# Performance work log

Hardware: AMD Instinct MI355X
Metric: run time of the kernel (lower is better)

Reference implementation:

```python
import jax, jax.numpy as jnp
import numpy as np

EMBED = 1024
FF = 4096
HEADS = 16
HEAD_SIZE = EMBED // HEADS


def setup_inputs() -> dict:
    key = jax.random.key(0)
    ks = jax.random.split(key, 12)
    s = 0.02
    inp = {
        "x": jax.random.normal(ks[0], (2, 2048, EMBED), dtype=jnp.float32),
        "Wq": jax.random.normal(ks[1], (EMBED, EMBED), dtype=jnp.float32) * s,
        "bq": jnp.zeros((EMBED,), jnp.float32),
        "Wk": jax.random.normal(ks[2], (EMBED, EMBED), dtype=jnp.float32) * s,
        "bk": jnp.zeros((EMBED,), jnp.float32),
        "Wv": jax.random.normal(ks[3], (EMBED, EMBED), dtype=jnp.float32) * s,
        "bv": jnp.zeros((EMBED,), jnp.float32),
        "Wo": jax.random.normal(ks[4], (EMBED, EMBED), dtype=jnp.float32) * s,
        "bo": jnp.zeros((EMBED,), jnp.float32),
        "W1": jax.random.normal(ks[5], (EMBED, FF), dtype=jnp.float32) * s,
        "b1": jnp.zeros((FF,), jnp.float32),
        "W2": jax.random.normal(ks[6], (FF, EMBED), dtype=jnp.float32) * s,
        "b2": jnp.zeros((EMBED,), jnp.float32),
        "ln1_g": jnp.ones((EMBED,), jnp.float32),
        "ln1_b": jnp.zeros((EMBED,), jnp.float32),
        "ln2_g": jnp.ones((EMBED,), jnp.float32),
        "ln2_b": jnp.zeros((EMBED,), jnp.float32),
    }
    return inp


def _layernorm(x, g, b, eps=1e-5):
    mu = jnp.mean(x, axis=-1, keepdims=True)
    var = jnp.var(x, axis=-1, keepdims=True)
    return (x - mu) * jax.lax.rsqrt(var + eps) * g + b


def _attn(x, Wq, bq, Wk, bk, Wv, bv, Wo, bo):
    B, S, E = x.shape
    q = (x @ Wq + bq).reshape(B, S, HEADS, HEAD_SIZE)
    k = (x @ Wk + bk).reshape(B, S, HEADS, HEAD_SIZE)
    v = (x @ Wv + bv).reshape(B, S, HEADS, HEAD_SIZE)
    # full (non-causal) attention, scores materialized as in the original
    att = jnp.einsum('bqhd,bkhd->bhqk', q, k) / jnp.sqrt(jnp.float32(HEAD_SIZE))
    att = jax.nn.softmax(att, axis=-1)
    out = jnp.einsum('bhqk,bkhd->bqhd', att, v).reshape(B, S, E)
    return out @ Wo + bo


def reference(x, Wq, bq, Wk, bk, Wv, bv, Wo, bo, W1, b1, W2, b2,
              ln1_g, ln1_b, ln2_g, ln2_b):
    x = x + _attn(_layernorm(x, ln1_g, ln1_b), Wq, bq, Wk, bk, Wv, bv, Wo, bo)
    h = _layernorm(x, ln2_g, ln2_b)
    x = x + (jax.nn.gelu(h @ W1 + b1) @ W2 + b2)
    return x
```

## Files before the change

kernel.cpp:

```cpp
#include <hip/hip_runtime.h>

typedef __bf16 bf16;
typedef __bf16 bf16x8 __attribute__((ext_vector_type(8)));
typedef __bf16 bf16x4 __attribute__((ext_vector_type(4)));
typedef float f32x4 __attribute__((ext_vector_type(4)));

#define EMBED 1024
#define FFDIM 4096
#define HEADS 16
#define HD 64
#define SEQ 2048
#define BATCH 2
#define TOKENS (BATCH * SEQ)
#define MB (1u << 20)


__device__ __forceinline__ void gld16(const void* g, void* l) {
  __builtin_amdgcn_global_load_lds(
      (const __attribute__((address_space(1))) void*)g,
      (__attribute__((address_space(3))) void*)l, 16, 0, 0);
}

__device__ __forceinline__ float gelu_f(float x) {
  float u = 0.7978845608028654f * (x + 0.044715f * x * x * x);
  float t = tanhf(u);
  return 0.5f * x * (1.0f + t);
}

__device__ __forceinline__ void xcd_tiles(int nx, int& tx, int& ty) {
  int lid = blockIdx.x + nx * blockIdx.y;
  tx = (lid >> 3) % nx;
  ty = ((lid / (8 * nx)) << 3) | (lid & 7);
}

__global__ __launch_bounds__(256) void transpose_cast(const float* __restrict__ in,
                                                      bf16* __restrict__ out,
                                                      int R, int C) {
  __shared__ float t[32][33];
  int bx = blockIdx.x * 32;
  int by = blockIdx.y * 32;
  int tx = threadIdx.x & 31;
  int ty = threadIdx.x >> 5;
#pragma unroll
  for (int i = 0; i < 32; i += 8)
    t[ty + i][tx] = in[(size_t)(by + ty + i) * C + bx + tx];
  __syncthreads();
#pragma unroll
  for (int i = 0; i < 32; i += 8)
    out[(size_t)(bx + ty + i) * R + by + tx] = (bf16)t[tx][ty + i];
}

__global__ __launch_bounds__(256) void ln_kernel(const float* __restrict__ x,
                                                 const float* __restrict__ g,
                                                 const float* __restrict__ b,
                                                 bf16* __restrict__ out) {
  int tok = blockIdx.x;
  int tid = threadIdx.x;
  const float4* xv = (const float4*)(x + (size_t)tok * EMBED);
  float4 v = xv[tid];
  float s = v.x + v.y + v.z + v.w;
  float s2 = v.x * v.x + v.y * v.y + v.z * v.z + v.w * v.w;
#pragma unroll
  for (int off = 32; off >= 1; off >>= 1) {
    s += __shfl_xor(s, off, 64);
    s2 += __shfl_xor(s2, off, 64);
  }
  __shared__ float ps[4], ps2[4];
  int w = tid >> 6;
  if ((tid & 63) == 0) { ps[w] = s; ps2[w] = s2; }
  __syncthreads();
  s = ps[0] + ps[1] + ps[2] + ps[3];
  s2 = ps2[0] + ps2[1] + ps2[2] + ps2[3];
  float mu = s * (1.0f / EMBED);
  float var = s2 * (1.0f / EMBED) - mu * mu;
  float r = rsqrtf(var + 1e-5f);
  float4 gg = ((const float4*)g)[tid];
  float4 bb = ((const float4*)b)[tid];
  bf16x4 o;
  o[0] = (bf16)((v.x - mu) * r * gg.x + bb.x);
  o[1] = (bf16)((v.y - mu) * r * gg.y + bb.y);
  o[2] = (bf16)((v.z - mu) * r * gg.z + bb.z);
  o[3] = (bf16)((v.w - mu) * r * gg.w + bb.w);
  ((bf16x4*)(out + (size_t)tok * EMBED))[tid] = o;
}

template <int MODE>
__global__ __launch_bounds__(256) void gemm_bt(const bf16* __restrict__ A,
                                               const bf16* __restrict__ BT,
                                               const float* __restrict__ bias,
                                               void* __restrict__ out,
                                               int M, int N, int K,
                                               const float* __restrict__ bias2,
                                               const float* __restrict__ bias3,
                                               void* __restrict__ out2,
                                               void* __restrict__ out3) {
  __shared__ bf16 ldsA[128 * 64];
  __shared__ bf16 ldsB[128 * 64];
  int tid = threadIdx.x;
  int wave = tid >> 6, lane = tid & 63;
  int lquad = lane >> 4, l15 = lane & 15;
  int wm = wave >> 1, wn = wave & 1;
  int tileM = blockIdx.y * 128, tileN = blockIdx.x * 128;

  f32x4 acc[4][4];
#pragma unroll
  for (int i = 0; i < 4; i++)
#pragma unroll
    for (int j = 0; j < 4; j++) acc[i][j] = (f32x4){0.f, 0.f, 0.f, 0.f};

  int srow = lane >> 3;
  int sch = lane & 7;

  for (int k0 = 0; k0 < K; k0 += 64) {
    __syncthreads();
#pragma unroll
    for (int c = 0; c < 4; c++) {
      int base = wave * 32 + c * 8;
      int row = base + srow;
      int ch = sch ^ (row & 7);
      gld16(&A[(size_t)(tileM + row) * K + k0 + ch * 8], &ldsA[base * 64]);
      gld16(&BT[(size_t)(tileN + row) * K + k0 + ch * 8], &ldsB[base * 64]);
    }
    __syncthreads();

    bf16x8 aF[2][4], bF[2][4];
#pragma unroll
    for (int ks = 0; ks < 2; ks++) {
#pragma unroll
      for (int i = 0; i < 4; i++) {
        int R = wm * 64 + i * 16 + l15;
        int ch = (ks * 4 + lquad) ^ (R & 7);
        aF[ks][i] = *(const bf16x8*)&ldsA[R * 64 + ch * 8];
      }
#pragma unroll
      for (int j = 0; j < 4; j++) {
        int R = wn * 64 + j * 16 + l15;
        int ch = (ks * 4 + lquad) ^ (R & 7);
        bF[ks][j] = *(const bf16x8*)&ldsB[R * 64 + ch * 8];
      }
    }
#pragma unroll
    for (int i = 0; i < 4; i++)
#pragma unroll
      for (int j = 0; j < 4; j++)
#pragma unroll
        for (int ks = 0; ks < 2; ks++)
          acc[i][j] = __builtin_amdgcn_mfma_f32_16x16x32_bf16(aF[ks][i], bF[ks][j], acc[i][j], 0, 0, 0);
  }

  int r0 = tileM + wm * 64;
  int c0 = tileN + wn * 64;
#pragma unroll
  for (int i = 0; i < 4; i++) {
#pragma unroll
    for (int j = 0; j < 4; j++) {
      int col = c0 + j * 16 + l15;
      float bv;
      if (MODE == 4) {
        int sel = col >> 10, cc = col & 1023;
        bv = (sel == 0 ? bias : sel == 1 ? bias2 : bias3)[cc];
      } else {
        bv = bias[col];
      }
#pragma unroll
      for (int r = 0; r < 4; r++) {
        int row = r0 + i * 16 + lquad * 4 + r;
        float v = acc[i][j][r] + bv;
        if (MODE == 0) {
          ((bf16*)out)[(size_t)row * N + col] = (bf16)v;
        } else if (MODE == 3) {
          ((bf16*)out)[(size_t)row * N + col] = (bf16)gelu_f(v);
        } else {
          int sel = col >> 10, cc = col & 1023;
          if (sel == 0) {
            ((bf16*)out)[(size_t)row * EMBED + cc] = (bf16)v;
          } else if (sel == 1) {
            ((bf16*)out2)[(size_t)row * EMBED + cc] = (bf16)v;
          } else {
            int bb = row >> 11, s = row & (SEQ - 1);
            ((bf16*)out3)[((size_t)(bb * EMBED + cc)) * SEQ + s] = (bf16)v;
          }
        }
      }
    }
  }
}

__global__ __launch_bounds__(256) void gemm_bt64(const bf16* __restrict__ A,
                                                 const bf16* __restrict__ BT,
                                                 const float* __restrict__ bias,
                                                 const float* __restrict__ res,
                                                 float* __restrict__ out,
                                                 int M, int N, int K) {
  __shared__ bf16 ldsA[128 * 64];
  __shared__ bf16 ldsB[64 * 64];
  int tid = threadIdx.x;
  int wave = tid >> 6, lane = tid & 63;
  int lquad = lane >> 4, l15 = lane & 15;
  int wm = wave >> 1, wn = wave & 1;
  int txs, tys;
  xcd_tiles(N >> 6, txs, tys);
  int tileM = tys * 128, tileN = txs * 64;

  f32x4 acc[4][2];
#pragma unroll
  for (int i = 0; i < 4; i++)
#pragma unroll
    for (int j = 0; j < 2; j++) acc[i][j] = (f32x4){0.f, 0.f, 0.f, 0.f};

  int srow = lane >> 3;
  int sch = lane & 7;

  for (int k0 = 0; k0 < K; k0 += 64) {
    __syncthreads();
#pragma unroll
    for (int c = 0; c < 4; c++) {
      int base = wave * 32 + c * 8;
      int row = base + srow;
      int ch = sch ^ (row & 7);
      gld16(&A[(size_t)(tileM + row) * K + k0 + ch * 8], &ldsA[base * 64]);
    }
#pragma unroll
    for (int c = 0; c < 2; c++) {
      int base = wave * 16 + c * 8;
      int row = base + srow;
      int ch = sch ^ (row & 7);
      gld16(&BT[(size_t)(tileN + row) * K + k0 + ch * 8], &ldsB[base * 64]);
    }
    __syncthreads();

    bf16x8 aF[2][4], bF[2][2];
#pragma unroll
    for (int ks = 0; ks < 2; ks++) {
#pragma unroll
      for (int i = 0; i < 4; i++) {
        int R = wm * 64 + i * 16 + l15;
        int ch = (ks * 4 + lquad) ^ (R & 7);
        aF[ks][i] = *(const bf16x8*)&ldsA[R * 64 + ch * 8];
      }
#pragma unroll
      for (int j = 0; j < 2; j++) {
        int R = wn * 32 + j * 16 + l15;
        int ch = (ks * 4 + lquad) ^ (R & 7);
        bF[ks][j] = *(const bf16x8*)&ldsB[R * 64 + ch * 8];
      }
    }
#pragma unroll
    for (int i = 0; i < 4; i++)
#pragma unroll
      for (int j = 0; j < 2; j++)
#pragma unroll
        for (int ks = 0; ks < 2; ks++)
          acc[i][j] = __builtin_amdgcn_mfma_f32_16x16x32_bf16(aF[ks][i], bF[ks][j], acc[i][j], 0, 0, 0);
  }

  int r0 = tileM + wm * 64;
  int c0 = tileN + wn * 32;
#pragma unroll
  for (int i = 0; i < 4; i++) {
#pragma unroll
    for (int j = 0; j < 2; j++) {
      int col = c0 + j * 16 + l15;
      float bv = bias[col];
#pragma unroll
      for (int r = 0; r < 4; r++) {
        int row = r0 + i * 16 + lquad * 4 + r;
        out[(size_t)row * N + col] = acc[i][j][r] + bv + res[(size_t)row * N + col];
      }
    }
  }
}

__global__ __launch_bounds__(256) void attn_kernel(const bf16* __restrict__ q,
                                                   const bf16* __restrict__ k,
                                                   const bf16* __restrict__ vT,
                                                   bf16* __restrict__ o) {
  int lid = blockIdx.x;
  int qb = (lid >> 3) & 31;
  int g = (lid & 7) | ((lid >> 8) << 3);
  int h = g & 15, b = g >> 4;
  int tid = threadIdx.x;
  int w = tid >> 6, lane = tid & 63;
  int lquad = lane >> 4, l15 = lane & 15;

  __shared__ bf16 ldsK[128 * 64];
  __shared__ bf16 ldsV[64 * 128];
  __shared__ bf16 ldsP[4][16 * 136];

  int qrow = b * SEQ + qb * 64 + w * 16 + l15;
  bf16x8 qB[2];
  qB[0] = *(const bf16x8*)&q[(size_t)qrow * EMBED + h * HD + 0 + lquad * 8];
  qB[1] = *(const bf16x8*)&q[(size_t)qrow * EMBED + h * HD + 32 + lquad * 8];

  f32x4 O[4];
#pragma unroll
  for (int j = 0; j < 4; j++) O[j] = (f32x4){0.f, 0.f, 0.f, 0.f};
  float m = -1e30f, lsum = 0.f;
  const float C2 = 0.18033688011112042f;

  for (int kb = 0; kb < SEQ; kb += 128) {
    __syncthreads();
#pragma unroll
    for (int c = 0; c < 4; c++) {
      int base = w * 32 + c * 8;
      int row = base + (lane >> 3);
      int ch = (lane & 7) ^ (row & 7);
      gld16(&k[(size_t)(b * SEQ + kb + row) * EMBED + h * HD + ch * 8],
            &ldsK[base * 64]);
    }
#pragma unroll
    for (int c = 0; c < 4; c++) {
      int base = w * 16 + c * 4;
      int row = base + (lane >> 4);
      int ch = (lane & 15) ^ (row & 7);
      gld16(&vT[(size_t)(b * EMBED + h * HD + row) * SEQ + kb + ch * 8],
            &ldsV[base * 128]);
    }
    __syncthreads();

    f32x4 st[8];
#pragma unroll
    for (int t = 0; t < 8; t++) {
      st[t] = (f32x4){0.f, 0.f, 0.f, 0.f};
#pragma unroll
      for (int ks = 0; ks < 2; ks++) {
        int R = t * 16 + l15;
        int ch = (ks * 4 + lquad) ^ (R & 7);
        bf16x8 kA = *(const bf16x8*)&ldsK[R * 64 + ch * 8];
        st[t] = __builtin_amdgcn_mfma_f32_16x16x32_bf16(kA, qB[ks], st[t], 0, 0, 0);
      }
    }

    float mt = fmaxf(fmaxf(st[0][0], st[0][1]), fmaxf(st[0][2], st[0][3]));
#pragma unroll
    for (int t = 1; t < 8; t++) {
      float a0 = fmaxf(st[t][0], st[t][1]);
      float a1 = fmaxf(st[t][2], st[t][3]);
      mt = fmaxf(mt, fmaxf(a0, a1));
    }
    mt = fmaxf(mt, __shfl_xor(mt, 16, 64));
    mt = fmaxf(mt, __shfl_xor(mt, 32, 64));
    float mn = fmaxf(m, mt);
    float alpha = __builtin_amdgcn_exp2f((m - mn) * C2);
    m = mn;
    float mc2 = m * C2;

    float rs = 0.f;
#pragma unroll
    for (int t = 0; t < 8; t++)
#pragma unroll
      for (int r = 0; r < 4; r++) {
        st[t][r] = __builtin_amdgcn_exp2f(fmaf(st[t][r], C2, -mc2));
        rs += st[t][r];
      }
    lsum = lsum * alpha + rs;
#pragma unroll
    for (int j = 0; j < 4; j++)
#pragma unroll
      for (int r = 0; r < 4; r++) O[j][r] *= alpha;

#pragma unroll
    for (int t = 0; t < 8; t++) {
      bf16x4 pk;
#pragma unroll
      for (int r = 0; r < 4; r++) pk[r] = (bf16)st[t][r];
      *(bf16x4*)&ldsP[w][l15 * 136 + t * 16 + lquad * 4] = pk;
    }
    bf16x8 pB[4];
#pragma unroll
    for (int ks2 = 0; ks2 < 4; ks2++)
      pB[ks2] = *(const bf16x8*)&ldsP[w][l15 * 136 + ks2 * 32 + lquad * 8];

#pragma unroll
    for (int j = 0; j < 4; j++) {
#pragma unroll
      for (int ks2 = 0; ks2 < 4; ks2++) {
        int R = j * 16 + l15;
        int ch = (ks2 * 4 + lquad) ^ (R & 7);
        bf16x8 vA = *(const bf16x8*)&ldsV[R * 128 + ch * 8];
        O[j] = __builtin_amdgcn_mfma_f32_16x16x32_bf16(vA, pB[ks2], O[j], 0, 0, 0);
      }
    }
  }

  lsum += __shfl_xor(lsum, 16, 64);
  lsum += __shfl_xor(lsum, 32, 64);
  float inv = 1.0f / lsum;
  int tok = b * SEQ + qb * 64 + w * 16 + l15;
#pragma unroll
  for (int j = 0; j < 4; j++) {
    bf16x4 ov;
#pragma unroll
    for (int r = 0; r < 4; r++) ov[r] = (bf16)(O[j][r] * inv);
    *(bf16x4*)&o[(size_t)tok * EMBED + h * HD + j * 16 + lquad * 4] = ov;
  }
}


extern "C" void kernel_launch(void* const* d_in, const int* in_sizes, int n_in,
                              void* d_out, int out_size, void* d_ws, size_t ws_size,
                              hipStream_t stream) {
  const float* x = (const float*)d_in[0];
  const float* Wq = (const float*)d_in[1];
  const float* bq = (const float*)d_in[2];
  const float* Wk = (const float*)d_in[3];
  const float* bk = (const float*)d_in[4];
  const float* Wv = (const float*)d_in[5];
  const float* bv = (const float*)d_in[6];
  const float* Wo = (const float*)d_in[7];
  const float* bo = (const float*)d_in[8];
  const float* W1 = (const float*)d_in[9];
  const float* b1 = (const float*)d_in[10];
  const float* W2 = (const float*)d_in[11];
  const float* b2 = (const float*)d_in[12];
  const float* ln1_g = (const float*)d_in[13];
  const float* ln1_b = (const float*)d_in[14];
  const float* ln2_g = (const float*)d_in[15];
  const float* ln2_b = (const float*)d_in[16];

  char* ws = (char*)d_ws;
  bf16* WqT = (bf16*)(ws + 0 * MB);
  bf16* WkT = (bf16*)(ws + 2 * MB);
  bf16* WvT = (bf16*)(ws + 4 * MB);
  bf16* WoT = (bf16*)(ws + 6 * MB);
  bf16* W1T = (bf16*)(ws + 8 * MB);
  bf16* W2T = (bf16*)(ws + 16 * MB);
  bf16* xn1 = (bf16*)(ws + 24 * MB);
  bf16* qbuf = (bf16*)(ws + 32 * MB);
  bf16* kbuf = (bf16*)(ws + 40 * MB);
  bf16* vT = (bf16*)(ws + 48 * MB);
  bf16* attnb = (bf16*)(ws + 56 * MB);
  float* x2f = (float*)(ws + 64 * MB);
  bf16* xn2 = (bf16*)(ws + 80 * MB);
  bf16* hb = (bf16*)(ws + 88 * MB);
  float* outf = (float*)d_out;

  transpose_cast<<<dim3(32, 32), 256, 0, stream>>>(Wq, WqT, EMBED, EMBED);
  transpose_cast<<<dim3(32, 32), 256, 0, stream>>>(Wk, WkT, EMBED, EMBED);
  transpose_cast<<<dim3(32, 32), 256, 0, stream>>>(Wv, WvT, EMBED, EMBED);
  transpose_cast<<<dim3(32, 32), 256, 0, stream>>>(Wo, WoT, EMBED, EMBED);
  transpose_cast<<<dim3(128, 32), 256, 0, stream>>>(W1, W1T, EMBED, FFDIM);
  transpose_cast<<<dim3(32, 128), 256, 0, stream>>>(W2, W2T, FFDIM, EMBED);

  ln_kernel<<<TOKENS, 256, 0, stream>>>(x, ln1_g, ln1_b, xn1);

  gemm_bt<4><<<dim3(3072 / 128, TOKENS / 128), 256, 0, stream>>>(
      xn1, WqT, bq, qbuf, TOKENS, 3072, EMBED, bk, bv, kbuf, vT);

  attn_kernel<<<dim3(SEQ / 64 * HEADS * BATCH), 256, 0, stream>>>(qbuf, kbuf, vT, attnb);

  gemm_bt64<<<dim3(EMBED / 64, TOKENS / 128), 256, 0, stream>>>(
      attnb, WoT, bo, x, x2f, TOKENS, EMBED, EMBED);

  ln_kernel<<<TOKENS, 256, 0, stream>>>(x2f, ln2_g, ln2_b, xn2);

  gemm_bt<3><<<dim3(FFDIM / 128, TOKENS / 128), 256, 0, stream>>>(
      xn2, W1T, b1, hb, TOKENS, FFDIM, EMBED,
      nullptr, nullptr, nullptr, nullptr);
  gemm_bt64<<<dim3(EMBED / 64, TOKENS / 128), 256, 0, stream>>>(
      hb, W2T, b2, x2f, outf, TOKENS, EMBED, FFDIM);
}
```

Before: 401.1 us.

## Process 128 queries per attention block and batch four weight transposes

The attention kernel now has each wave handle two 16-row query fragments (128 queries per block). Each K/V tile loaded into LDS is therefore reused across twice as many queries, halving K/V global traffic and LDS fills per query. The cost is more registers per thread (double accumulators and scores) and a larger P buffer in LDS, which may reduce occupancy, and the grid shrinks to 512 blocks. Separately, the four square weight transposes are merged into one launch to cut launch overhead.

New measurement: 407.5 us. Within noise of the previous version (+1.6%).

```diff
diff --git a/kernel.cpp b/kernel.cpp
--- a/kernel.cpp
+++ b/kernel.cpp
@@ -48,6 +48,32 @@
 #pragma unroll
   for (int i = 0; i < 32; i += 8)
     out[(size_t)(bx + ty + i) * R + by + tx] = (bf16)t[tx][ty + i];
+}
+
+__global__ __launch_bounds__(256) void transpose_cast4(
+    const float* __restrict__ W0, const float* __restrict__ W1,
+    const float* __restrict__ W2, const float* __restrict__ W3,
+    bf16* __restrict__ O0, bf16* __restrict__ O1,
+    bf16* __restrict__ O2, bf16* __restrict__ O3) {
+  const float* in;
+  bf16* out;
+  int z = blockIdx.z;
+  if (z == 0) { in = W0; out = O0; }
+  else if (z == 1) { in = W1; out = O1; }
+  else if (z == 2) { in = W2; out = O2; }
+  else { in = W3; out = O3; }
+  __shared__ float t[32][33];
+  int bx = blockIdx.x * 32;
+  int by = blockIdx.y * 32;
+  int tx = threadIdx.x & 31;
+  int ty = threadIdx.x >> 5;
+#pragma unroll
+  for (int i = 0; i < 32; i += 8)
+    t[ty + i][tx] = in[(size_t)(by + ty + i) * EMBED + bx + tx];
+  __syncthreads();
+#pragma unroll
+  for (int i = 0; i < 32; i += 8)
+    out[(size_t)(bx + ty + i) * EMBED + by + tx] = (bf16)t[tx][ty + i];
 }
 
 __global__ __launch_bounds__(256) void ln_kernel(const float* __restrict__ x,
@@ -276,8 +302,8 @@
                                                    const bf16* __restrict__ vT,
                                                    bf16* __restrict__ o) {
   int lid = blockIdx.x;
-  int qb = (lid >> 3) & 31;
-  int g = (lid & 7) | ((lid >> 8) << 3);
+  int qb = (lid >> 3) & 15;
+  int g = (lid & 7) | ((lid >> 7) << 3);
   int h = g & 15, b = g >> 4;
   int tid = threadIdx.x;
   int w = tid >> 6, lane = tid & 63;
@@ -285,17 +311,22 @@
 
   __shared__ bf16 ldsK[128 * 64];
   __shared__ bf16 ldsV[64 * 128];
-  __shared__ bf16 ldsP[4][16 * 136];
-
-  int qrow = b * SEQ + qb * 64 + w * 16 + l15;
-  bf16x8 qB[2];
-  qB[0] = *(const bf16x8*)&q[(size_t)qrow * EMBED + h * HD + 0 + lquad * 8];
-  qB[1] = *(const bf16x8*)&q[(size_t)qrow * EMBED + h * HD + 32 + lquad * 8];
-
-  f32x4 O[4];
-#pragma unroll
-  for (int j = 0; j < 4; j++) O[j] = (f32x4){0.f, 0.f, 0.f, 0.f};
-  float m = -1e30f, lsum = 0.f;
+  __shared__ bf16 ldsP[4][32 * 136];
+
+  bf16x8 qB[2][2];
+#pragma unroll
+  for (int f = 0; f < 2; f++) {
+    int qrow = b * SEQ + qb * 128 + w * 32 + f * 16 + l15;
+    qB[f][0] = *(const bf16x8*)&q[(size_t)qrow * EMBED + h * HD + lquad * 8];
+    qB[f][1] = *(const bf16x8*)&q[(size_t)qrow * EMBED + h * HD + 32 + lquad * 8];
+  }
+
+  f32x4 O[2][4];
+#pragma unroll
+  for (int f = 0; f < 2; f++)
+#pragma unroll
+    for (int j = 0; j < 4; j++) O[f][j] = (f32x4){0.f, 0.f, 0.f, 0.f};
+  float m[2] = {-1e30f, -1e30f}, lsum[2] = {0.f, 0.f};
   const float C2 = 0.18033688011112042f;
 
   for (int kb = 0; kb < SEQ; kb += 128) {
@@ -318,58 +349,66 @@
     }
     __syncthreads();
 
-    f32x4 st[8];
+    f32x4 st[2][8];
 #pragma unroll
     for (int t = 0; t < 8; t++) {
-      st[t] = (f32x4){0.f, 0.f, 0.f, 0.f};
+      st[0][t] = (f32x4){0.f, 0.f, 0.f, 0.f};
+      st[1][t] = (f32x4){0.f, 0.f, 0.f, 0.f};
 #pragma unroll
       for (int ks = 0; ks < 2; ks++) {
         int R = t * 16 + l15;
         int ch = (ks * 4 + lquad) ^ (R & 7);
         bf16x8 kA = *(const bf16x8*)&ldsK[R * 64 + ch * 8];
-        st[t] = __builtin_amdgcn_mfma_f32_16x16x32_bf16(kA, qB[ks], st[t], 0, 0, 0);
-      }
-    }
-
-    float mt = fmaxf(fmaxf(st[0][0], st[0][1]), fmaxf(st[0][2], st[0][3]));
-#pragma unroll
-    for (int t = 1; t < 8; t++) {
-      float a0 = fmaxf(st[t][0], st[t][1]);
-      float a1 = fmaxf(st[t][2], st[t][3]);
-      mt = fmaxf(mt, fmaxf(a0, a1));
-    }
-    mt = fmaxf(mt, __shfl_xor(mt, 16, 64));
-    mt = fmaxf(mt, __shfl_xor(mt, 32, 64));
-    float mn = fmaxf(m, mt);
-    float alpha = __builtin_amdgcn_exp2f((m - mn) * C2);
-    m = mn;
-    float mc2 = m * C2;
-
-    float rs = 0.f;
-#pragma unroll
-    for (int t = 0; t < 8; t++)
-#pragma unroll
-      for (int r = 0; r < 4; r++) {
-        st[t][r] = __builtin_amdgcn_exp2f(fmaf(st[t][r], C2, -mc2));
-        rs += st[t][r];
-      }
-    lsum = lsum * alpha + rs;
-#pragma unroll
-    for (int j = 0; j < 4; j++)
-#pragma unroll
-      for (int r = 0; r < 4; r++) O[j][r] *= alpha;
-
-#pragma unroll
-    for (int t = 0; t < 8; t++) {
-      bf16x4 pk;
-#pragma unroll
-      for (int r = 0; r < 4; r++) pk[r] = (bf16)st[t][r];
-      *(bf16x4*)&ldsP[w][l15 * 136 + t * 16 + lquad * 4] = pk;
-    }
-    bf16x8 pB[4];
-#pragma unroll
-    for (int ks2 = 0; ks2 < 4; ks2++)
-      pB[ks2] = *(const bf16x8*)&ldsP[w][l15 * 136 + ks2 * 32 + lquad * 8];
+        st[0][t] = __builtin_amdgcn_mfma_f32_16x16x32_bf16(kA, qB[0][ks], st[0][t], 0, 0, 0);
+        st[1][t] = __builtin_amdgcn_mfma_f32_16x16x32_bf16(kA, qB[1][ks], st[1][t], 0, 0, 0);
+      }
+    }
+
+#pragma unroll
+    for (int f = 0; f < 2; f++) {
+      float mt = fmaxf(fmaxf(st[f][0][0], st[f][0][1]), fmaxf(st[f][0][2], st[f][0][3]));
+#pragma unroll
+      for (int t = 1; t < 8; t++) {
+        float a0 = fmaxf(st[f][t][0], st[f][t][1]);
+        float a1 = fmaxf(st[f][t][2], st[f][t][3]);
+        mt = fmaxf(mt, fmaxf(a0, a1));
+      }
+      mt = fmaxf(mt, __shfl_xor(mt, 16, 64));
+      mt = fmaxf(mt, __shfl_xor(mt, 32, 64));
+      float mn = fmaxf(m[f], mt);
+      float alpha = __builtin_amdgcn_exp2f((m[f] - mn) * C2);
+      m[f] = mn;
+      float mc2 = mn * C2;
+
+      float rs = 0.f;
+#pragma unroll
+      for (int t = 0; t < 8; t++)
+#pragma unroll
+        for (int r = 0; r < 4; r++) {
+          st[f][t][r] = __builtin_amdgcn_exp2f(fmaf(st[f][t][r], C2, -mc2));
+          rs += st[f][t][r];
+        }
+      lsum[f] = lsum[f] * alpha + rs;
+#pragma unroll
+      for (int j = 0; j < 4; j++)
+#pragma unroll
+        for (int r = 0; r < 4; r++) O[f][j][r] *= alpha;
+
+#pragma unroll
+      for (int t = 0; t < 8; t++) {
+        bf16x4 pk;
+#pragma unroll
+        for (int r = 0; r < 4; r++) pk[r] = (bf16)st[f][t][r];
+        *(bf16x4*)&ldsP[w][(f * 16 + l15) * 136 + t * 16 + lquad * 4] = pk;
+      }
+    }
+
+    bf16x8 pB[2][4];
+#pragma unroll
+    for (int f = 0; f < 2; f++)
+#pragma unroll
+      for (int ks2 = 0; ks2 < 4; ks2++)
+        pB[f][ks2] = *(const bf16x8*)&ldsP[w][(f * 16 + l15) * 136 + ks2 * 32 + lquad * 8];
 
 #pragma unroll
     for (int j = 0; j < 4; j++) {
@@ -378,21 +417,26 @@
         int R = j * 16 + l15;
         int ch = (ks2 * 4 + lquad) ^ (R & 7);
         bf16x8 vA = *(const bf16x8*)&ldsV[R * 128 + ch * 8];
-        O[j] = __builtin_amdgcn_mfma_f32_16x16x32_bf16(vA, pB[ks2], O[j], 0, 0, 0);
-      }
-    }
-  }
-
-  lsum += __shfl_xor(lsum, 16, 64);
-  lsum += __shfl_xor(lsum, 32, 64);
-  float inv = 1.0f / lsum;
-  int tok = b * SEQ + qb * 64 + w * 16 + l15;
-#pragma unroll
-  for (int j = 0; j < 4; j++) {
-    bf16x4 ov;
-#pragma unroll
-    for (int r = 0; r < 4; r++) ov[r] = (bf16)(O[j][r] * inv);
-    *(bf16x4*)&o[(size_t)tok * EMBED + h * HD + j * 16 + lquad * 4] = ov;
+        O[0][j] = __builtin_amdgcn_mfma_f32_16x16x32_bf16(vA, pB[0][ks2], O[0][j], 0, 0, 0);
+        O[1][j] = __builtin_amdgcn_mfma_f32_16x16x32_bf16(vA, pB[1][ks2], O[1][j], 0, 0, 0);
+      }
+    }
+  }
+
+#pragma unroll
+  for (int f = 0; f < 2; f++) {
+    float ls = lsum[f];
+    ls += __shfl_xor(ls, 16, 64);
+    ls += __shfl_xor(ls, 32, 64);
+    float inv = 1.0f / ls;
+    int tok = b * SEQ + qb * 128 + w * 32 + f * 16 + l15;
+#pragma unroll
+    for (int j = 0; j < 4; j++) {
+      bf16x4 ov;
+#pragma unroll
+      for (int r = 0; r < 4; r++) ov[r] = (bf16)(O[f][j][r] * inv);
+      *(bf16x4*)&o[(size_t)tok * EMBED + h * HD + j * 16 + lquad * 4] = ov;
+    }
   }
 }
 
@@ -435,10 +479,8 @@
   bf16* hb = (bf16*)(ws + 88 * MB);
   float* outf = (float*)d_out;
 
-  transpose_cast<<<dim3(32, 32), 256, 0, stream>>>(Wq, WqT, EMBED, EMBED);
-  transpose_cast<<<dim3(32, 32), 256, 0, stream>>>(Wk, WkT, EMBED, EMBED);
-  transpose_cast<<<dim3(32, 32), 256, 0, stream>>>(Wv, WvT, EMBED, EMBED);
-  transpose_cast<<<dim3(32, 32), 256, 0, stream>>>(Wo, WoT, EMBED, EMBED);
+  transpose_cast4<<<dim3(32, 32, 4), 256, 0, stream>>>(Wq, Wk, Wv, Wo,
+                                                       WqT, WkT, WvT, WoT);
   transpose_cast<<<dim3(128, 32), 256, 0, stream>>>(W1, W1T, EMBED, FFDIM);
   transpose_cast<<<dim3(32, 128), 256, 0, stream>>>(W2, W2T, FFDIM, EMBED);
 
@@ -447,7 +489,7 @@
   gemm_bt<4><<<dim3(3072 / 128, TOKENS / 128), 256, 0, stream>>>(
       xn1, WqT, bq, qbuf, TOKENS, 3072, EMBED, bk, bv, kbuf, vT);
 
-  attn_kernel<<<dim3(SEQ / 64 * HEADS * BATCH), 256, 0, stream>>>(qbuf, kbuf, vT, attnb);
+  attn_kernel<<<dim3(SEQ / 128 * HEADS * BATCH), 256, 0, stream>>>(qbuf, kbuf, vT, attnb);
 
   gemm_bt64<<<dim3(EMBED / 64, TOKENS / 128), 256, 0, stream>>>(
       attnb, WoT, bo, x, x2f, TOKENS, EMBED, EMBED);
```
